# Kernel tuning notes

Measured on AMD Instinct MI355X. Metric: run time of the kernel, lower is better.

Reference implementation:

```python
import jax, jax.numpy as jnp
import numpy as np

K = 3        # kernel_size
STRIDE = 1
PAD = 1
BASIS = 8    # act_fun.get_size()


def cheb_basis(x):
    """Chebyshev polynomial basis T_0..T_{BASIS-1} of tanh(x); appends basis axis."""
    t = jnp.tanh(x)
    polys = [jnp.ones_like(t), t]
    for _ in range(BASIS - 2):
        polys.append(2.0 * t * polys[-1] - polys[-2])
    return jnp.stack(polys, axis=-1)  # (..., BASIS)


def silu(x):
    return x * jax.nn.sigmoid(x)


def unfold(x):
    """torch F.unfold equivalent: (b,c,h,w) -> (b, c, K*K, L), L = ho*wo."""
    b, c, h, w = x.shape
    ho = (h - K + 2 * PAD) // STRIDE + 1
    wo = (w - K + 2 * PAD) // STRIDE + 1
    xp = jnp.pad(x, ((0, 0), (0, 0), (PAD, PAD), (PAD, PAD)))
    pats = [xp[:, :, i:i + STRIDE * ho:STRIDE, j:j + STRIDE * wo:STRIDE]
            for i in range(K) for j in range(K)]
    pats = jnp.stack(pats, axis=2)  # (b, c, K*K, ho, wo)
    return pats.reshape(b, c, K * K, ho * wo), ho, wo


def setup_inputs() -> dict:
    key = jax.random.key(0)
    k1, k2, k3 = jax.random.split(key, 3)
    cin, cout = 64, 64
    x = jax.random.normal(k1, (16, cin, 32, 32), dtype=jnp.float32)
    # xavier_normal_ on (in,out,k^2,1): std = sqrt(2/(fan_in+fan_out)) approx
    w = jax.random.normal(k2, (cin, cout, K * K), dtype=jnp.float32) * jnp.sqrt(2.0 / (cin + cout))
    # normal_(c, 0, 0.1) on (in,out,k^2,1,basis) -> squeeze the broadcast dim
    c = jax.random.normal(k3, (cin, cout, K * K, BASIS), dtype=jnp.float32) * 0.1
    return {"x": x, "w": w, "c": c}


def reference(x, w, c):
    b = x.shape[0]
    pats, ho, wo = unfold(x)          # (b, i, k, l)
    res = silu(pats)                  # residual activation path
    act = cheb_basis(pats)            # (b, i, k, l, s) spline basis
    # sum_i sum_k w[i,o,k] * res[b,i,k,l]
    term1 = jnp.einsum('iok,bikl->bol', w, res)
    # sum_i sum_k sum_s w[i,o,k]*c[i,o,k,s]*act[b,i,k,l,s] (fused, avoids (b,i,o,k,l,s))
    cw = c * w[..., None]             # (i, o, k, s)
    term2 = jnp.einsum('ioks,bikls->bol', cw, act)
    return (term1 + term2).reshape(b, -1, ho, wo)
```

## Files before the change

kernel.cpp:

```cpp
#include <hip/hip_runtime.h>
#include <hip/hip_bf16.h>


#define CIN   64
#define COUT  64
#define HW    32
#define LL    1024
#define NS    8

typedef __attribute__((ext_vector_type(8))) short short8;
typedef __attribute__((ext_vector_type(4))) float f32x4;


__global__ void prep_kernel(const float* __restrict__ w,
                            const float* __restrict__ c,
                            __hip_bfloat16* __restrict__ Wt,
                            float* __restrict__ bias,
                            const float* __restrict__ x,
                            float* __restrict__ dummy) {
    const int bx = blockIdx.x;
    if (bx < 144) {
        const int tid = bx * 256 + threadIdx.x;
        const int i = tid / (9 * COUT);
        const int r = tid - i * 9 * COUT;
        const int k = r / COUT;
        const int o = r - k * COUT;
        const int widx = (i * COUT + o) * 9 + k;
        const float wv = w[widx];
        __hip_bfloat16* dst = Wt + (size_t)tid * NS;
        dst[0] = __float2bfloat16(wv);
#pragma unroll
        for (int s = 1; s < 8; ++s) dst[s] = __float2bfloat16(wv * c[widx * 8 + s]);
        return;
    }
    if (bx < 208) {
        const int o = bx - 144;
        const int i = threadIdx.x;
        if (i >= 64) return;
        float v = 0.f;
#pragma unroll
        for (int k = 0; k < 9; ++k) {
            const int idx = (i * COUT + o) * 9 + k;
            v += w[idx] * c[idx * 8];
        }
#pragma unroll
        for (int off = 32; off > 0; off >>= 1) v += __shfl_down(v, off);
        if (i == 0) bias[o] = v;
        return;
    }
    const int idx = bx - 208;
    const int r  = idx & 7;
    const int m  = idx >> 3;
    const int b  = r + 8 * (m & 1);
    const int ch = m >> 1;
    const float4 v = ((const float4*)(x + (size_t)(b * CIN + ch) * LL))[threadIdx.x];
    const float acc = v.x + v.y + v.z + v.w;
    if (acc == 1.0e-37f) dummy[threadIdx.x] = acc;
}

__global__ __launch_bounds__(1024, 4) void kan_fused_kernel(
        const float* __restrict__ x,
        const __hip_bfloat16* __restrict__ Wt,
        const float* __restrict__ bias,
        float* __restrict__ out) {
    __shared__ __align__(16) unsigned short Wlds[52224];

    const int tid   = threadIdx.x;
    const int wv    = tid >> 6;
    const int lane  = tid & 63;
    const int quad  = lane >> 4;
    const int l16   = lane & 15;
    const int kq    = wv >> 2;
    const int oq    = wv & 3;

    const int b    = blockIdx.x;
    const int row0 = blockIdx.y << 1;

    const unsigned short* WtU = (const unsigned short*)Wt;
    float* xf = (float*)Wlds;

#pragma unroll
    for (int p = 0; p < 9; ++p) {
        const int cell = p * 1024 + tid;
        if (cell < 8704) {
            const int ch  = cell / 136;
            const int pos = cell - ch * 136;
            const int r4  = pos / 34;
            const int col = pos - r4 * 34;
            const int gy  = row0 - 1 + r4;
            const int gx  = col - 1;
            float v = 0.f;
            if ((unsigned)gy < 32u && (unsigned)gx < 32u)
                v = x[((size_t)(b * CIN + ch) * HW + gy) * HW + gx];
            xf[cell] = v;
        }
    }
    __syncthreads();

    f32x4 acc[4];
#pragma unroll
    for (int h = 0; h < 4; ++h) acc[h] = (f32x4){0.f, 0.f, 0.f, 0.f};

    for (int chunk = 0; chunk < 4; ++chunk) {
        const int chbase = kq * 16 + chunk * 4;
        unsigned short* usd = Wlds + 17408 + (chunk & 1) * 17408 + kq * 4352;

#pragma unroll
        for (int p = 0; p < 3; ++p) {
            const int cell = (p * 4 + oq) * 64 + lane;
            if (cell < 544) {
                const int ch  = cell & 3;
                const int pos = cell >> 2;
                const float xv = xf[(chbase + ch) * 136 + pos];
                const float e   = __expf(xv);
                const float sig = e * __builtin_amdgcn_rcpf(1.f + e);
                const float res = xv * sig;
                const float t   = 1.f - 2.f * __builtin_amdgcn_rcpf(__builtin_fmaf(e, e, 1.f));
                const float t2  = t + t;
                const float T2 = __builtin_fmaf(t2, t,  -1.f);
                const float T3 = __builtin_fmaf(t2, T2, -t);
                const float T4 = __builtin_fmaf(t2, T3, -T2);
                const float T5 = __builtin_fmaf(t2, T4, -T3);
                const float T6 = __builtin_fmaf(t2, T5, -T4);
                const float T7 = __builtin_fmaf(t2, T6, -T5);
                union { __hip_bfloat162 h2[4]; float4 f4; } U;
                U.h2[0] = __float22bfloat162_rn(make_float2(res, t));
                U.h2[1] = __float22bfloat162_rn(make_float2(T2, T3));
                U.h2[2] = __float22bfloat162_rn(make_float2(T4, T5));
                U.h2[3] = __float22bfloat162_rn(make_float2(T6, T7));
                *(float4*)(usd + cell * 8) = U.f4;
            }
        }
        __syncthreads();

        const unsigned short* wchunk = WtU +
            ((size_t)(chbase + quad) * 9 * COUT + (oq << 4) + l16) * NS;
#pragma unroll
        for (int kpos = 0; kpos < 9; ++kpos) {
            const int dy = kpos / 3 - 1, dx = kpos % 3 - 1;
            const int posb = (dy + 1) * 34 + (dx + 1);
            short8 af0 = *(const short8*)(usd + (((posb      + l16) * 4 + quad)) * 8);
            short8 af1 = *(const short8*)(usd + (((posb + 16 + l16) * 4 + quad)) * 8);
            short8 af2 = *(const short8*)(usd + (((posb + 34 + l16) * 4 + quad)) * 8);
            short8 af3 = *(const short8*)(usd + (((posb + 50 + l16) * 4 + quad)) * 8);
            short8 wf = *(const short8*)(wchunk + kpos * COUT * NS);
            acc[0] = __builtin_amdgcn_mfma_f32_16x16x32_bf16(wf, af0, acc[0], 0, 0, 0);
            acc[1] = __builtin_amdgcn_mfma_f32_16x16x32_bf16(wf, af1, acc[1], 0, 0, 0);
            acc[2] = __builtin_amdgcn_mfma_f32_16x16x32_bf16(wf, af2, acc[2], 0, 0, 0);
            acc[3] = __builtin_amdgcn_mfma_f32_16x16x32_bf16(wf, af3, acc[3], 0, 0, 0);
        }
    }

    float* red = (float*)Wlds;
#pragma unroll
    for (int h = 0; h < 4; ++h)
#pragma unroll
        for (int r = 0; r < 4; ++r) {
            const int p = h * 16 + l16;
            const int o = (oq << 4) + quad * 4 + r;
            red[(kq * 64 + p) * 65 + o] = acc[h][r];
        }
    __syncthreads();

#pragma unroll
    for (int rep = 0; rep < 4; ++rep) {
        const int v = rep * 1024 + tid;
        const int p = v & 63;
        const int o = v >> 6;
        const float s = red[p * 65 + o] + red[(64 + p) * 65 + o]
                      + red[(128 + p) * 65 + o] + red[(192 + p) * 65 + o] + bias[o];
        out[(size_t)(b * COUT + o) * LL + (row0 + (p >> 5)) * HW + (p & 31)] = s;
    }
}

extern "C" void kernel_launch(void* const* d_in, const int* in_sizes, int n_in,
                              void* d_out, int out_size, void* d_ws, size_t ws_size,
                              hipStream_t stream) {
    const float* x = (const float*)d_in[0];
    const float* w = (const float*)d_in[1];
    const float* c = (const float*)d_in[2];
    float* out = (float*)d_out;

    char* ws = (char*)d_ws;
    __hip_bfloat16* Wt    = (__hip_bfloat16*)(ws);
    float*          bias  = (float*)(ws + 589824);
    float*          dummy = (float*)(ws + 590080);

    prep_kernel<<<1232, 256, 0, stream>>>(w, c, Wt, bias, x, dummy);
    kan_fused_kernel<<<dim3(16, 16), 1024, 0, stream>>>(x, Wt, bias, out);
}
```

Measured before the change: 74.10 us.

## Split output channels across grid z and stream x loads directly into registers

The fused KAN conv kernel now splits the 64 output channels into two halves across blockIdx.z, which doubles the grid to 512 blocks. Each wave handles one 16-channel output half and one pixel row, with two accumulators instead of four. The fp32 input staging tile in LDS is removed: each thread loads its x values straight from global memory into registers, prefetching the next channel chunk while the current chunk's activations are stored. This shrinks LDS per block and raises the launch-bounds occupancy hint, aiming at more parallelism and latency hiding. The cost is that the Chebyshev activation work and the x loads are duplicated across the two output-half blocks.

```diff
diff --git a/kernel.cpp b/kernel.cpp
--- a/kernel.cpp
+++ b/kernel.cpp
@@ -58,12 +58,12 @@
     if (acc == 1.0e-37f) dummy[threadIdx.x] = acc;
 }
 
-__global__ __launch_bounds__(1024, 4) void kan_fused_kernel(
+__global__ __launch_bounds__(1024, 8) void kan_fused_kernel(
         const float* __restrict__ x,
         const __hip_bfloat16* __restrict__ Wt,
         const float* __restrict__ bias,
         float* __restrict__ out) {
-    __shared__ __align__(16) unsigned short Wlds[52224];
+    __shared__ __align__(16) unsigned short Wlds[34816];
 
     const int tid   = threadIdx.x;
     const int wv    = tid >> 6;
@@ -71,105 +71,109 @@
     const int quad  = lane >> 4;
     const int l16   = lane & 15;
     const int kq    = wv >> 2;
-    const int oq    = wv & 3;
+    const int wq    = wv & 3;
+    const int oh    = wq & 1;
+    const int ph    = wq >> 1;
 
     const int b    = blockIdx.x;
     const int row0 = blockIdx.y << 1;
+    const int ohB  = blockIdx.z;
 
     const unsigned short* WtU = (const unsigned short*)Wt;
-    float* xf = (float*)Wlds;
 
-#pragma unroll
-    for (int p = 0; p < 9; ++p) {
-        const int cell = p * 1024 + tid;
-        if (cell < 8704) {
-            const int ch  = cell / 136;
-            const int pos = cell - ch * 136;
-            const int r4  = pos / 34;
-            const int col = pos - r4 * 34;
-            const int gy  = row0 - 1 + r4;
-            const int gx  = col - 1;
-            float v = 0.f;
-            if ((unsigned)gy < 32u && (unsigned)gx < 32u)
-                v = x[((size_t)(b * CIN + ch) * HW + gy) * HW + gx];
-            xf[cell] = v;
-        }
-    }
-    __syncthreads();
+    const int cell0 = wq * 64 + lane;
+    const int cell1 = cell0 + 256;
+    const bool has2 = (wq == 0) & (lane < 32);
+    const int cell2 = 512 + lane;
 
-    f32x4 acc[4];
-#pragma unroll
-    for (int h = 0; h < 4; ++h) acc[h] = (f32x4){0.f, 0.f, 0.f, 0.f};
+    auto loadx = [&](int cell, int chunk) -> float {
+        const int ch  = cell & 3;
+        const int pos = cell >> 2;
+        const int r4  = pos / 34;
+        const int col = pos - r4 * 34;
+        const int gy  = row0 - 1 + r4;
+        const int gx  = col - 1;
+        float v = 0.f;
+        if ((unsigned)gy < 32u && (unsigned)gx < 32u)
+            v = x[((size_t)(b * CIN + kq * 16 + chunk * 4 + ch) * HW + gy) * HW + gx];
+        return v;
+    };
+
+    f32x4 acc[2];
+    acc[0] = (f32x4){0.f, 0.f, 0.f, 0.f};
+    acc[1] = (f32x4){0.f, 0.f, 0.f, 0.f};
+
+    float xv0 = loadx(cell0, 0);
+    float xv1 = loadx(cell1, 0);
+    float xv2 = has2 ? loadx(cell2, 0) : 0.f;
 
     for (int chunk = 0; chunk < 4; ++chunk) {
-        const int chbase = kq * 16 + chunk * 4;
-        unsigned short* usd = Wlds + 17408 + (chunk & 1) * 17408 + kq * 4352;
+        unsigned short* usd = Wlds + (chunk & 1) * 17408 + kq * 4352;
 
-#pragma unroll
-        for (int p = 0; p < 3; ++p) {
-            const int cell = (p * 4 + oq) * 64 + lane;
-            if (cell < 544) {
-                const int ch  = cell & 3;
-                const int pos = cell >> 2;
-                const float xv = xf[(chbase + ch) * 136 + pos];
-                const float e   = __expf(xv);
-                const float sig = e * __builtin_amdgcn_rcpf(1.f + e);
-                const float res = xv * sig;
-                const float t   = 1.f - 2.f * __builtin_amdgcn_rcpf(__builtin_fmaf(e, e, 1.f));
-                const float t2  = t + t;
-                const float T2 = __builtin_fmaf(t2, t,  -1.f);
-                const float T3 = __builtin_fmaf(t2, T2, -t);
-                const float T4 = __builtin_fmaf(t2, T3, -T2);
-                const float T5 = __builtin_fmaf(t2, T4, -T3);
-                const float T6 = __builtin_fmaf(t2, T5, -T4);
-                const float T7 = __builtin_fmaf(t2, T6, -T5);
-                union { __hip_bfloat162 h2[4]; float4 f4; } U;
-                U.h2[0] = __float22bfloat162_rn(make_float2(res, t));
-                U.h2[1] = __float22bfloat162_rn(make_float2(T2, T3));
-                U.h2[2] = __float22bfloat162_rn(make_float2(T4, T5));
-                U.h2[3] = __float22bfloat162_rn(make_float2(T6, T7));
-                *(float4*)(usd + cell * 8) = U.f4;
-            }
+        auto actstore = [&](int cell, float xvv) {
+            const float e   = __expf(xvv);
+            const float sig = e * __builtin_amdgcn_rcpf(1.f + e);
+            const float res = xvv * sig;
+            const float t   = 1.f - 2.f * __builtin_amdgcn_rcpf(__builtin_fmaf(e, e, 1.f));
+            const float t2  = t + t;
+            const float T2 = __builtin_fmaf(t2, t,  -1.f);
+            const float T3 = __builtin_fmaf(t2, T2, -t);
+            const float T4 = __builtin_fmaf(t2, T3, -T2);
+            const float T5 = __builtin_fmaf(t2, T4, -T3);
+            const float T6 = __builtin_fmaf(t2, T5, -T4);
+            const float T7 = __builtin_fmaf(t2, T6, -T5);
+            union { __hip_bfloat162 h2[4]; float4 f4; } U;
+            U.h2[0] = __float22bfloat162_rn(make_float2(res, t));
+            U.h2[1] = __float22bfloat162_rn(make_float2(T2, T3));
+            U.h2[2] = __float22bfloat162_rn(make_float2(T4, T5));
+            U.h2[3] = __float22bfloat162_rn(make_float2(T6, T7));
+            *(float4*)(usd + cell * 8) = U.f4;
+        };
+        actstore(cell0, xv0);
+        actstore(cell1, xv1);
+        if (has2) actstore(cell2, xv2);
+
+        if (chunk < 3) {
+            xv0 = loadx(cell0, chunk + 1);
+            xv1 = loadx(cell1, chunk + 1);
+            xv2 = has2 ? loadx(cell2, chunk + 1) : 0.f;
         }
         __syncthreads();
 
         const unsigned short* wchunk = WtU +
-            ((size_t)(chbase + quad) * 9 * COUT + (oq << 4) + l16) * NS;
+            ((size_t)(kq * 16 + chunk * 4 + quad) * 9 * COUT + ohB * 32 + oh * 16 + l16) * NS;
 #pragma unroll
         for (int kpos = 0; kpos < 9; ++kpos) {
             const int dy = kpos / 3 - 1, dx = kpos % 3 - 1;
-            const int posb = (dy + 1) * 34 + (dx + 1);
-            short8 af0 = *(const short8*)(usd + (((posb      + l16) * 4 + quad)) * 8);
-            short8 af1 = *(const short8*)(usd + (((posb + 16 + l16) * 4 + quad)) * 8);
-            short8 af2 = *(const short8*)(usd + (((posb + 34 + l16) * 4 + quad)) * 8);
-            short8 af3 = *(const short8*)(usd + (((posb + 50 + l16) * 4 + quad)) * 8);
+            const int posb = (ph + dy + 1) * 34 + (dx + 1);
+            short8 af0 = *(const short8*)(usd + ((posb      + l16) * 4 + quad) * 8);
+            short8 af1 = *(const short8*)(usd + ((posb + 16 + l16) * 4 + quad) * 8);
             short8 wf = *(const short8*)(wchunk + kpos * COUT * NS);
             acc[0] = __builtin_amdgcn_mfma_f32_16x16x32_bf16(wf, af0, acc[0], 0, 0, 0);
             acc[1] = __builtin_amdgcn_mfma_f32_16x16x32_bf16(wf, af1, acc[1], 0, 0, 0);
-            acc[2] = __builtin_amdgcn_mfma_f32_16x16x32_bf16(wf, af2, acc[2], 0, 0, 0);
-            acc[3] = __builtin_amdgcn_mfma_f32_16x16x32_bf16(wf, af3, acc[3], 0, 0, 0);
         }
     }
 
     float* red = (float*)Wlds;
 #pragma unroll
-    for (int h = 0; h < 4; ++h)
+    for (int h = 0; h < 2; ++h)
 #pragma unroll
         for (int r = 0; r < 4; ++r) {
-            const int p = h * 16 + l16;
-            const int o = (oq << 4) + quad * 4 + r;
-            red[(kq * 64 + p) * 65 + o] = acc[h][r];
+            const int p = ph * 32 + h * 16 + l16;
+            const int o = oh * 16 + quad * 4 + r;
+            red[(kq * 64 + p) * 33 + o] = acc[h][r];
         }
     __syncthreads();
 
 #pragma unroll
-    for (int rep = 0; rep < 4; ++rep) {
+    for (int rep = 0; rep < 2; ++rep) {
         const int v = rep * 1024 + tid;
         const int p = v & 63;
         const int o = v >> 6;
-        const float s = red[p * 65 + o] + red[(64 + p) * 65 + o]
-                      + red[(128 + p) * 65 + o] + red[(192 + p) * 65 + o] + bias[o];
-        out[(size_t)(b * COUT + o) * LL + (row0 + (p >> 5)) * HW + (p & 31)] = s;
+        const float s = red[p * 33 + o] + red[(64 + p) * 33 + o]
+                      + red[(128 + p) * 33 + o] + red[(192 + p) * 33 + o]
+                      + bias[ohB * 32 + o];
+        out[(size_t)(b * COUT + ohB * 32 + o) * LL + (row0 + (p >> 5)) * HW + (p & 31)] = s;
     }
 }
 
@@ -187,5 +191,5 @@
     float*          dummy = (float*)(ws + 590080);
 
     prep_kernel<<<1232, 256, 0, stream>>>(w, c, Wt, bias, x, dummy);
-    kan_fused_kernel<<<dim3(16, 16), 1024, 0, stream>>>(x, Wt, bias, out);
+    kan_fused_kernel<<<dim3(16, 16, 2), 1024, 0, stream>>>(x, Wt, bias, out);
 }
```

New measurement: 78.06 us. +5.3%, slower.

## Switch to 32x32x16 MFMA tiles with 8-way channel split across waves

Applied to the files above, without the earlier changes.

Replaces the 16x16x32 bf16 MFMA tiling with 32x32x16 MFMAs. Each wave now owns 32 output pixels and all 64 output channels, using two accumulators, and the input channels are split eight ways across waves instead of four. The basis-expansion stage is redistributed so that all threads fill the shared activation buffer cooperatively. The final reduction now sums eight partials in two halves to fit the shared memory. The aim is fewer MFMA issues and fewer LDS fragment loads per FLOP, at the cost of a larger cross-wave reduction and an extra barrier.

```diff
diff --git a/kernel.cpp b/kernel.cpp
--- a/kernel.cpp
+++ b/kernel.cpp
@@ -9,7 +9,7 @@
 #define NS    8
 
 typedef __attribute__((ext_vector_type(8))) short short8;
-typedef __attribute__((ext_vector_type(4))) float f32x4;
+typedef __attribute__((ext_vector_type(16))) float f32x16;
 
 
 __global__ void prep_kernel(const float* __restrict__ w,
@@ -65,13 +65,13 @@
         float* __restrict__ out) {
     __shared__ __align__(16) unsigned short Wlds[52224];
 
-    const int tid   = threadIdx.x;
-    const int wv    = tid >> 6;
-    const int lane  = tid & 63;
-    const int quad  = lane >> 4;
-    const int l16   = lane & 15;
-    const int kq    = wv >> 2;
-    const int oq    = wv & 3;
+    const int tid  = threadIdx.x;
+    const int wv   = tid >> 6;
+    const int lane = tid & 63;
+    const int l31  = lane & 31;
+    const int half = lane >> 5;
+    const int kq   = wv >> 1;
+    const int pm   = wv & 1;
 
     const int b    = blockIdx.x;
     const int row0 = blockIdx.y << 1;
@@ -97,79 +97,80 @@
     }
     __syncthreads();
 
-    f32x4 acc[4];
+    f32x16 acc0, acc1;
 #pragma unroll
-    for (int h = 0; h < 4; ++h) acc[h] = (f32x4){0.f, 0.f, 0.f, 0.f};
+    for (int r = 0; r < 16; ++r) { acc0[r] = 0.f; acc1[r] = 0.f; }
+
+    const size_t wlane = ((size_t)(kq * 8 + half) * 9 * 64 + l31) * 8;
 
     for (int chunk = 0; chunk < 4; ++chunk) {
-        const int chbase = kq * 16 + chunk * 4;
-        unsigned short* usd = Wlds + 17408 + (chunk & 1) * 17408 + kq * 4352;
+        unsigned short* ubuf = Wlds + 17408 + (chunk & 1) * 17408;
 
-#pragma unroll
-        for (int p = 0; p < 3; ++p) {
-            const int cell = (p * 4 + oq) * 64 + lane;
-            if (cell < 544) {
-                const int ch  = cell & 3;
-                const int pos = cell >> 2;
-                const float xv = xf[(chbase + ch) * 136 + pos];
-                const float e   = __expf(xv);
-                const float sig = e * __builtin_amdgcn_rcpf(1.f + e);
-                const float res = xv * sig;
-                const float t   = 1.f - 2.f * __builtin_amdgcn_rcpf(__builtin_fmaf(e, e, 1.f));
-                const float t2  = t + t;
-                const float T2 = __builtin_fmaf(t2, t,  -1.f);
-                const float T3 = __builtin_fmaf(t2, T2, -t);
-                const float T4 = __builtin_fmaf(t2, T3, -T2);
-                const float T5 = __builtin_fmaf(t2, T4, -T3);
-                const float T6 = __builtin_fmaf(t2, T5, -T4);
-                const float T7 = __builtin_fmaf(t2, T6, -T5);
-                union { __hip_bfloat162 h2[4]; float4 f4; } U;
-                U.h2[0] = __float22bfloat162_rn(make_float2(res, t));
-                U.h2[1] = __float22bfloat162_rn(make_float2(T2, T3));
-                U.h2[2] = __float22bfloat162_rn(make_float2(T4, T5));
-                U.h2[3] = __float22bfloat162_rn(make_float2(T6, T7));
-                *(float4*)(usd + cell * 8) = U.f4;
-            }
-        }
+        auto doCell = [&](int cell) {
+            const int kqc = cell / 272;
+            const int rr  = cell - kqc * 272;
+            const int chl = rr & 1;
+            const int pos = rr >> 1;
+            const float xv = xf[(kqc * 8 + chunk * 2 + chl) * 136 + pos];
+            const float e   = __expf(xv);
+            const float sig = e * __builtin_amdgcn_rcpf(1.f + e);
+            const float res = xv * sig;
+            const float t   = 1.f - 2.f * __builtin_amdgcn_rcpf(__builtin_fmaf(e, e, 1.f));
+            const float t2  = t + t;
+            const float T2 = __builtin_fmaf(t2, t,  -1.f);
+            const float T3 = __builtin_fmaf(t2, T2, -t);
+            const float T4 = __builtin_fmaf(t2, T3, -T2);
+            const float T5 = __builtin_fmaf(t2, T4, -T3);
+            const float T6 = __builtin_fmaf(t2, T5, -T4);
+            const float T7 = __builtin_fmaf(t2, T6, -T5);
+            union { __hip_bfloat162 h2[4]; float4 f4; } U;
+            U.h2[0] = __float22bfloat162_rn(make_float2(res, t));
+            U.h2[1] = __float22bfloat162_rn(make_float2(T2, T3));
+            U.h2[2] = __float22bfloat162_rn(make_float2(T4, T5));
+            U.h2[3] = __float22bfloat162_rn(make_float2(T6, T7));
+            *(float4*)(ubuf + cell * 8) = U.f4;
+        };
+        doCell(tid);
+        doCell(tid + 1024);
+        if (tid < 128) doCell(tid + 2048);
+
         __syncthreads();
 
-        const unsigned short* wchunk = WtU +
-            ((size_t)(chbase + quad) * 9 * COUT + (oq << 4) + l16) * NS;
+        const unsigned short* afb = ubuf + kq * 2176;
+        const unsigned short* wc  = WtU + wlane + (size_t)chunk * 9216;
 #pragma unroll
         for (int kpos = 0; kpos < 9; ++kpos) {
-            const int dy = kpos / 3 - 1, dx = kpos % 3 - 1;
-            const int posb = (dy + 1) * 34 + (dx + 1);
-            short8 af0 = *(const short8*)(usd + (((posb      + l16) * 4 + quad)) * 8);
-            short8 af1 = *(const short8*)(usd + (((posb + 16 + l16) * 4 + quad)) * 8);
-            short8 af2 = *(const short8*)(usd + (((posb + 34 + l16) * 4 + quad)) * 8);
-            short8 af3 = *(const short8*)(usd + (((posb + 50 + l16) * 4 + quad)) * 8);
-            short8 wf = *(const short8*)(wchunk + kpos * COUT * NS);
-            acc[0] = __builtin_amdgcn_mfma_f32_16x16x32_bf16(wf, af0, acc[0], 0, 0, 0);
-            acc[1] = __builtin_amdgcn_mfma_f32_16x16x32_bf16(wf, af1, acc[1], 0, 0, 0);
-            acc[2] = __builtin_amdgcn_mfma_f32_16x16x32_bf16(wf, af2, acc[2], 0, 0, 0);
-            acc[3] = __builtin_amdgcn_mfma_f32_16x16x32_bf16(wf, af3, acc[3], 0, 0, 0);
+            const int posb = (pm + kpos / 3) * 34 + (kpos % 3);
+            short8 af  = *(const short8*)(afb + ((posb + l31) * 2 + half) * 8);
+            short8 wf0 = *(const short8*)(wc + kpos * 512);
+            short8 wf1 = *(const short8*)(wc + kpos * 512 + 256);
+            acc0 = __builtin_amdgcn_mfma_f32_32x32x16_bf16(wf0, af, acc0, 0, 0, 0);
+            acc1 = __builtin_amdgcn_mfma_f32_32x32x16_bf16(wf1, af, acc1, 0, 0, 0);
         }
     }
 
     float* red = (float*)Wlds;
 #pragma unroll
-    for (int h = 0; h < 4; ++h)
+    for (int h = 0; h < 2; ++h) {
+        if (h) __syncthreads();
+        const f32x16 a = h ? acc1 : acc0;
 #pragma unroll
-        for (int r = 0; r < 4; ++r) {
-            const int p = h * 16 + l16;
-            const int o = (oq << 4) + quad * 4 + r;
-            red[(kq * 64 + p) * 65 + o] = acc[h][r];
+        for (int r = 0; r < 16; ++r) {
+            const int ol = (r & 3) + 8 * (r >> 2) + 4 * half;
+            red[(kq * 64 + pm * 32 + l31) * 33 + ol] = a[r];
         }
-    __syncthreads();
-
+        __syncthreads();
 #pragma unroll
-    for (int rep = 0; rep < 4; ++rep) {
-        const int v = rep * 1024 + tid;
-        const int p = v & 63;
-        const int o = v >> 6;
-        const float s = red[p * 65 + o] + red[(64 + p) * 65 + o]
-                      + red[(128 + p) * 65 + o] + red[(192 + p) * 65 + o] + bias[o];
-        out[(size_t)(b * COUT + o) * LL + (row0 + (p >> 5)) * HW + (p & 31)] = s;
+        for (int rep = 0; rep < 2; ++rep) {
+            const int v  = rep * 1024 + tid;
+            const int p  = v & 63;
+            const int ol = v >> 6;
+            float s = bias[h * 32 + ol];
+#pragma unroll
+            for (int kqq = 0; kqq < 8; ++kqq)
+                s += red[(kqq * 64 + p) * 33 + ol];
+            out[(size_t)(b * COUT + h * 32 + ol) * LL + (row0 + (p >> 5)) * HW + (p & 31)] = s;
+        }
     }
 }
 
```

New measurement: 76.20 us. +2.8%, slower.
